# Kernel tuning notes

Measured on AMD Instinct MI355X. Metric: run time of the kernel, lower is better.

The kernel has to match this reference:

```python
import jax, jax.numpy as jnp
import numpy as np

B, T, D, H, O = 64, 512, 512, 1024, 512

def _xavier(key, shape):
    fan_out, fan_in = shape
    limit = np.sqrt(6.0 / (fan_in + fan_out))
    return jax.random.uniform(key, shape, jnp.float32, -limit, limit)

def setup_inputs() -> dict:
    key = jax.random.key(0)
    k_in, k_wx, k_wh, k_wo = jax.random.split(key, 4)
    inputs = jax.random.normal(k_in, (B, T, D), dtype=jnp.float32)
    Wx = _xavier(k_wx, (3 * H, D))   # x2h weight (n*H, D)
    bx = jnp.zeros((3 * H,), jnp.float32)
    Wh = _xavier(k_wh, (3 * H, H))   # h2h weight (n*H, H)
    bh = jnp.zeros((3 * H,), jnp.float32)
    Wo = _xavier(k_wo, (O, H))       # output head
    bo = jnp.zeros((O,), jnp.float32)
    return {"inputs": inputs, "Wx": Wx, "bx": bx, "Wh": Wh, "bh": bh, "Wo": Wo, "bo": bo}

def _gru(inputs, Wx, bx, Wh, bh):
    # precompute input projection for all timesteps: (B, T, 3H)
    x_all = jnp.einsum('btd,gd->btg', inputs, Wx) + bx

    def step(h, x_t):
        # h: (B, H); x_t: (B, 3H)
        h_proj = h @ Wh.T + bh                  # (B, 3H)
        x_r, x_u, x_n = jnp.split(x_t, 3, axis=-1)
        h_r, h_u, h_n = jnp.split(h_proj, 3, axis=-1)
        reset = jax.nn.sigmoid(x_r + h_r)
        upd = jax.nn.sigmoid(x_u + h_u)
        new = jnp.tanh(x_n + reset * h_n)       # activation='tanh'
        hy = upd * h + (1.0 - upd) * new
        return hy, hy

    h0 = jnp.zeros((inputs.shape[0], Wh.shape[1]), inputs.dtype)
    _, hs = jax.lax.scan(step, h0, jnp.swapaxes(x_all, 0, 1))  # hs: (T, B, H)
    return jnp.swapaxes(hs, 0, 1)               # (B, T, H)

def reference(inputs, Wx, bx, Wh, bh, Wo, bo):
    hiddens = _gru(inputs, Wx, bx, Wh, bh)       # (B, T, H)
    out = jnp.einsum('bth,oh->bto', hiddens, Wo) + bo  # (B, T, O)
    return hiddens, out
```

## Files before the change

kernel.cpp:

```cpp
#include <hip/hip_runtime.h>
#include <hip/hip_bf16.h>

typedef __attribute__((ext_vector_type(8))) short short8;
typedef __attribute__((ext_vector_type(4))) float float4v;

__device__ __forceinline__ float bf2f(short b) {
    unsigned u = ((unsigned)(unsigned short)b) << 16;
    union { unsigned u; float f; } c; c.u = u; return c.f;
}
__device__ __forceinline__ short f2bf(float f) {
    union { float f; unsigned u; } c; c.f = f;
    unsigned r = 0x7FFFu + ((c.u >> 16) & 1u);
    return (short)((c.u + r) >> 16);
}
__device__ __forceinline__ float ldf(const void* p, size_t i, bool f32) {
    return f32 ? ((const float*)p)[i] : bf2f(((const short*)p)[i]);
}
__device__ __forceinline__ short8 frag8(const void* p, size_t i, bool f32) {
    short8 r;
    if (f32) {
        const float* q = (const float*)p + i;
#pragma unroll
        for (int j = 0; j < 8; j++) r[j] = f2bf(q[j]);
    } else {
        r = *(const short8*)((const short*)p + i);
    }
    return r;
}

__global__ __launch_bounds__(256) void dpm_spin(const float* __restrict__ seed,
                                               float* __restrict__ sink, int iters)
{
    float a = seed[threadIdx.x & 15];
    float b = seed[(threadIdx.x & 15) + 16];
    a = (a > 2.f || a < -2.f || (a < 0.01f && a > -0.01f)) ? 1.0000001f : a;
    float x = b + 1.f;
    int n = iters * 16;
#pragma unroll 16
    for (int i = 0; i < n; i++) x = __builtin_fmaf(x, a, b);
    if (x == 12345.6789f) sink[(((size_t)blockIdx.x * 256 + threadIdx.x) & 65535)] = x;
}

__global__ void detect_dtype(const unsigned short* __restrict__ in, unsigned* __restrict__ flag)
{
    int t = threadIdx.x;
    int sane = 0;
    for (int i = t; i < 256; i += 64) {
        unsigned e = (in[i] >> 7) & 0xFF;
        sane += (e >= 0x70 && e <= 0x8A) ? 1 : 0;
    }
#pragma unroll
    for (int o = 32; o > 0; o >>= 1) sane += __shfl_down(sane, o);
    if (t == 0) *flag = (sane >= 200) ? 0u : 1u;
}

__global__ void init_scratch(short* __restrict__ hb, unsigned* __restrict__ cnt)
{
    int i = blockIdx.x * 256 + threadIdx.x;
    if (i < 4 * 65536) hb[i] = 0;
    if (i < 512) cnt[i] = 0;
}

__global__ __launch_bounds__(256, 1) void gemm_bt(
    const void* __restrict__ A, const void* __restrict__ B,
    const void* __restrict__ bias, void* __restrict__ outbase, size_t coff,
    const unsigned* __restrict__ flag, int M, int N, int K)
{
    const bool f32 = flag && (flag[0] != 0u);
    __shared__ short Ah[128][72], Bh[128][72];
    __shared__ short Al[128][72], Bl[128][72];
    const int tid  = threadIdx.x;
    const int wid  = tid >> 6;
    const int lane = tid & 63;
    const int ln = lane & 15, q = lane >> 4;
    const int bm = blockIdx.x * 128, bn = blockIdx.y * 128;
    const int wm = (wid & 1) * 64, wn = (wid >> 1) * 64;

    float4v acc[4][4];
#pragma unroll
    for (int i = 0; i < 4; i++)
#pragma unroll
        for (int j = 0; j < 4; j++) acc[i][j] = (float4v){0.f, 0.f, 0.f, 0.f};

    for (int k0 = 0; k0 < K; k0 += 64) {
#pragma unroll
        for (int c = 0; c < 4; c++) {
            int chunk = tid + c * 256;
            int row = chunk >> 3;
            int kq  = (chunk & 7) * 8;
            size_t ga = (size_t)(bm + row) * K + k0 + kq;
            size_t gb = (size_t)(bn + row) * K + k0 + kq;
            if (f32) {
                const float* Af = (const float*)A;
                const float* Bf = (const float*)B;
#pragma unroll
                for (int j = 0; j < 8; j++) {
                    float av = Af[ga + j], bv = Bf[gb + j];
                    short ah = f2bf(av), bh = f2bf(bv);
                    Ah[row][kq + j] = ah; Al[row][kq + j] = f2bf(av - bf2f(ah));
                    Bh[row][kq + j] = bh; Bl[row][kq + j] = f2bf(bv - bf2f(bh));
                }
            } else {
                *(short8*)&Ah[row][kq] = *(const short8*)((const short*)A + ga);
                *(short8*)&Bh[row][kq] = *(const short8*)((const short*)B + gb);
            }
        }
        __syncthreads();
#pragma unroll
        for (int kt = 0; kt < 2; kt++) {
            short8 avh[4], bvh[4];
#pragma unroll
            for (int i = 0; i < 4; i++) avh[i] = *(const short8*)&Ah[wm + i * 16 + ln][kt * 32 + q * 8];
#pragma unroll
            for (int j = 0; j < 4; j++) bvh[j] = *(const short8*)&Bh[wn + j * 16 + ln][kt * 32 + q * 8];
#pragma unroll
            for (int i = 0; i < 4; i++)
#pragma unroll
                for (int j = 0; j < 4; j++)
                    acc[i][j] = __builtin_amdgcn_mfma_f32_16x16x32_bf16(avh[i], bvh[j], acc[i][j], 0, 0, 0);
            if (f32) {
                short8 avl[4], bvl[4];
#pragma unroll
                for (int i = 0; i < 4; i++) avl[i] = *(const short8*)&Al[wm + i * 16 + ln][kt * 32 + q * 8];
#pragma unroll
                for (int j = 0; j < 4; j++) bvl[j] = *(const short8*)&Bl[wn + j * 16 + ln][kt * 32 + q * 8];
#pragma unroll
                for (int i = 0; i < 4; i++)
#pragma unroll
                    for (int j = 0; j < 4; j++) {
                        acc[i][j] = __builtin_amdgcn_mfma_f32_16x16x32_bf16(avh[i], bvl[j], acc[i][j], 0, 0, 0);
                        acc[i][j] = __builtin_amdgcn_mfma_f32_16x16x32_bf16(avl[i], bvh[j], acc[i][j], 0, 0, 0);
                    }
            }
        }
        __syncthreads();
    }
#pragma unroll
    for (int j = 0; j < 4; j++) {
        int col = bn + wn + j * 16 + ln;
        float bvv = ldf(bias, col, f32);
#pragma unroll
        for (int i = 0; i < 4; i++) {
#pragma unroll
            for (int r = 0; r < 4; r++) {
                int row = bm + wm + i * 16 + q * 4 + r;
                size_t idx = coff + (size_t)row * N + col;
                float v = acc[i][j][r] + bvv;
                if (f32) ((float*)outbase)[idx] = v;
                else     ((short*)outbase)[idx] = f2bf(v);
            }
        }
    }
}

#define NWG 256
__global__ __launch_bounds__(192, 1) void gru_rec(
    const void* __restrict__ inputs,
    const void* __restrict__ Wx,
    const void* __restrict__ bx,
    const void* __restrict__ Wh,
    const void* __restrict__ bh,
    short* __restrict__ hb,
    unsigned* __restrict__ cnt,
    const unsigned* __restrict__ flag,
    void* __restrict__ hid)
{
    const bool f32 = flag && (flag[0] != 0u);
    __shared__ short xs[8192];
    __shared__ short hs[2][16384];
    __shared__ float Px[3][16][17];
    __shared__ float Ph[3][16][17];
    __shared__ float hown[16][17];
    __shared__ float bxs[3][16], bhs[3][16];

    const int tid  = threadIdx.x;
    const int w    = blockIdx.x;
    const int gb   = w >> 6;
    const int c    = w & 63;
    const int g    = tid >> 6;
    const int lane = tid & 63;
    const int ln   = lane & 15, q = lane >> 4;

    const size_t whbase = (size_t)(g * 1024 + c * 16 + ln) * 1024;
    short8 wf[32];
#pragma unroll
    for (int kt = 0; kt < 32; kt++) wf[kt] = frag8(Wh, whbase + kt * 32 + q * 8, f32);

    const size_t wxbase = (size_t)(g * 1024 + c * 16 + ln) * 512;
    short8 wxf[16];
#pragma unroll
    for (int kt = 0; kt < 16; kt++) wxf[kt] = frag8(Wx, wxbase + kt * 32 + q * 8, f32);

    for (int e = tid; e < 256; e += 192) hown[e >> 4][e & 15] = 0.f;
    if (tid < 48) {
        int gg = tid >> 4, jj = tid & 15;
        bxs[gg][jj] = ldf(bx, gg * 1024 + c * 16 + jj, f32);
        bhs[gg][jj] = ldf(bh, gg * 1024 + c * 16 + jj, f32);
    }
    __syncthreads();

    for (int t = 0; t < 512; t++) {
        const short* hsrc = hb + (size_t)((t & 1) ? 2 : 0) * 65536 + gb * 16384;
        short*       hdst = hb + (size_t)((t & 1) ? 0 : 2) * 65536 + gb * 16384;

        float4v ax = (float4v){0.f,0.f,0.f,0.f};
        float4v ah = (float4v){0.f,0.f,0.f,0.f};

        unsigned long long rv[11][2];
        auto load_chunk = [&](int pl) {
            const short* src_ = hsrc + pl * 65536;
#pragma unroll
            for (int i = 0; i < 11; i++) { int e = tid + i * 192; if (e < 2048) {
                const unsigned long long* p_ = (const unsigned long long*)(src_ + e * 8);
                rv[i][0] = __hip_atomic_load(p_,     __ATOMIC_RELAXED, __HIP_MEMORY_SCOPE_AGENT);
                rv[i][1] = __hip_atomic_load(p_ + 1, __ATOMIC_RELAXED, __HIP_MEMORY_SCOPE_AGENT);
            } }
        };
        auto write_chunk = [&](int d) {
#pragma unroll
            for (int i = 0; i < 11; i++) { int e = tid + i * 192; if (e < 2048) {
                int kb = e >> 4, r = e & 15;
                union { unsigned long long qq[2]; short8 v; } u_;
                u_.qq[0] = rv[i][0]; u_.qq[1] = rv[i][1];
                *(short8*)((char*)&hs[d][0] + (kb << 8) + ((r ^ (kb & 15)) << 4)) = u_.v;
            } }
        };

#pragma unroll 4
        for (int i = 0; i < 6; i++) { int e = tid + i * 192; if (e < 1024) {
            int kb = e & 63, r = e >> 6;
            size_t gi = (size_t)(gb * 16 + r) * 262144 + (size_t)t * 512 + kb * 8;
            short8 v = frag8(inputs, gi, f32);
            *(short8*)((char*)xs + (kb << 8) + ((r ^ (kb & 15)) << 4)) = v;
        } }
        __syncthreads();

        if (t) {
            if (tid < 64) {
                const unsigned* fp = &cnt[((t - 1) & 1) * 256 + gb * 64 + tid];
                while (__hip_atomic_load(fp, __ATOMIC_RELAXED, __HIP_MEMORY_SCOPE_AGENT) < (unsigned)t)
                    __builtin_amdgcn_s_sleep(2);
            }
            __syncthreads();
        }

        load_chunk(0);
#pragma unroll
        for (int kt = 0; kt < 16; kt++) {
            int kb = kt * 4 + q;
            short8 a = *(const short8*)((const char*)xs + (kb << 8) + ((ln ^ (kb & 15)) << 4));
            ax = __builtin_amdgcn_mfma_f32_16x16x32_bf16(a, wxf[kt], ax, 0, 0, 0);
        }
        write_chunk(0);
        __syncthreads();

        load_chunk(1);
#pragma unroll
        for (int kt = 0; kt < 32; kt++) {
            int kb = kt * 4 + q;
            short8 a = *(const short8*)((const char*)&hs[0][0] + (kb << 8) + ((ln ^ (kb & 15)) << 4));
            ah = __builtin_amdgcn_mfma_f32_16x16x32_bf16(a, wf[kt], ah, 0, 0, 0);
        }
        write_chunk(1);
        __syncthreads();
#pragma unroll
        for (int kt = 0; kt < 32; kt++) {
            int kb = kt * 4 + q;
            short8 a = *(const short8*)((const char*)&hs[1][0] + (kb << 8) + ((ln ^ (kb & 15)) << 4));
            ah = __builtin_amdgcn_mfma_f32_16x16x32_bf16(a, wf[kt], ah, 0, 0, 0);
        }

#pragma unroll
        for (int r = 0; r < 4; r++) {
            Px[g][q * 4 + r][ln] = ax[r];
            Ph[g][q * 4 + r][ln] = ah[r];
        }
        __syncthreads();

        for (int e = tid; e < 256; e += 192) {
            int r = e >> 4, jj = e & 15;
            float xr = Px[0][r][jj] + bxs[0][jj];
            float xu = Px[1][r][jj] + bxs[1][jj];
            float xn = Px[2][r][jj] + bxs[2][jj];
            float pr = Ph[0][r][jj] + bhs[0][jj];
            float pu = Ph[1][r][jj] + bhs[1][jj];
            float pn = Ph[2][r][jj] + bhs[2][jj];
            float rg = 1.f / (1.f + __expf(-(xr + pr)));
            float ug = 1.f / (1.f + __expf(-(xu + pu)));
            float ng = tanhf(xn + rg * pn);
            float hy = ug * hown[r][jj] + (1.f - ug) * ng;
            hown[r][jj] = hy;
            size_t b = (size_t)(gb * 16 + r);
            size_t hidx = (b * 512 + t) * 1024 + c * 16 + jj;
            if (f32) ((float*)hid)[hidx] = hy;
            else     ((short*)hid)[hidx] = f2bf(hy);
        }
        __syncthreads();

        if (tid < 64) {
            int r = tid & 15, kbl = (tid >> 4) & 1, pl = (tid >> 5) & 1;
            union { unsigned long long qq[2]; short8 v; } u;
#pragma unroll
            for (int j = 0; j < 8; j++) {
                float hy = hown[r][kbl * 8 + j];
                short hh = f2bf(hy);
                u.v[j] = pl ? f2bf(hy - bf2f(hh)) : hh;
            }
            unsigned long long* dp = (unsigned long long*)
                (hdst + (size_t)pl * 65536 + (size_t)(2 * c + kbl) * 128 + r * 8);
            __hip_atomic_store(dp,     u.qq[0], __ATOMIC_RELAXED, __HIP_MEMORY_SCOPE_AGENT);
            __hip_atomic_store(dp + 1, u.qq[1], __ATOMIC_RELAXED, __HIP_MEMORY_SCOPE_AGENT);
        }
        asm volatile("s_waitcnt vmcnt(0)" ::: "memory");
        __syncthreads();

        if (tid == 0)
            __hip_atomic_store(&cnt[(t & 1) * 256 + gb * 64 + c], (unsigned)(t + 1),
                               __ATOMIC_RELAXED, __HIP_MEMORY_SCOPE_AGENT);
    }
}

extern "C" void kernel_launch(void* const* d_in, const int* in_sizes, int n_in,
                              void* d_out, int out_size, void* d_ws, size_t ws_size,
                              hipStream_t stream)
{
    const void* inputs = d_in[0];
    const void* Wx     = d_in[1];
    const void* bx     = d_in[2];
    const void* Wh     = d_in[3];
    const void* bh     = d_in[4];
    const void* Wo     = d_in[5];
    const void* bo     = d_in[6];

    const size_t HID_ELEMS = (size_t)64 * 512 * 1024;

    short* hb; unsigned* cnt; unsigned* flag;
    const bool use_ws = (d_ws != nullptr) && (ws_size >= (size_t)(4096 + 4 * 65536 * 2));
    if (use_ws) {
        cnt  = (unsigned*)d_ws;
        flag = cnt + 512;
        hb   = (short*)((char*)d_ws + 4096);
    } else {
        short* outh = (short*)d_out + HID_ELEMS;
        hb   = outh;
        cnt  = (unsigned*)(outh + 4 * 65536);
        flag = nullptr;
    }

    if (use_ws) detect_dtype<<<1, 64, 0, stream>>>((const unsigned short*)inputs, flag);
    init_scratch<<<1024, 256, 0, stream>>>(hb, cnt);

    gru_rec<<<NWG, 192, 0, stream>>>(inputs, Wx, bx, Wh, bh, hb, cnt, flag, d_out);

    dpm_spin<<<2048, 256, 0, stream>>>((const float*)Wx, (float*)hb, 7032);

    gemm_bt<<<dim3(256, 4), 256, 0, stream>>>(d_out, Wo, bo, d_out, HID_ELEMS, flag, 32768, 512, 1024);
}
```

Before: 5.791 ms.

## Split GRU recurrence across 512 workgroups with 8 batch rows each and drop the spin kernel

The persistent recurrent kernel now gives each workgroup 8 batch rows instead of 16 and launches 512 workgroups, two per CU. The aim is more parallel resources per timestep and less LDS per block. Barriers are consolidated: the x-tile load and the peer-wait share one barrier, and the h chunks are loaded once into registers. A single counter buffer replaces the double-buffered one, and the trailing barrier before the flag store is removed. The unrelated dummy FMA spin kernel launched between the recurrence and the output GEMM is deleted. Risks: the 16-row MFMAs now carry half-padded rows, and all 512 workgroups must be co-resident for the spin-wait synchronization to make progress.

```diff
diff --git a/kernel.cpp b/kernel.cpp
--- a/kernel.cpp
+++ b/kernel.cpp
@@ -20,25 +20,14 @@
     short8 r;
     if (f32) {
         const float* q = (const float*)p + i;
-#pragma unroll
-        for (int j = 0; j < 8; j++) r[j] = f2bf(q[j]);
+        float4v a = *(const float4v*)q;
+        float4v b = *(const float4v*)(q + 4);
+#pragma unroll
+        for (int j = 0; j < 4; j++) { r[j] = f2bf(a[j]); r[4 + j] = f2bf(b[j]); }
     } else {
         r = *(const short8*)((const short*)p + i);
     }
     return r;
-}
-
-__global__ __launch_bounds__(256) void dpm_spin(const float* __restrict__ seed,
-                                               float* __restrict__ sink, int iters)
-{
-    float a = seed[threadIdx.x & 15];
-    float b = seed[(threadIdx.x & 15) + 16];
-    a = (a > 2.f || a < -2.f || (a < 0.01f && a > -0.01f)) ? 1.0000001f : a;
-    float x = b + 1.f;
-    int n = iters * 16;
-#pragma unroll 16
-    for (int i = 0; i < n; i++) x = __builtin_fmaf(x, a, b);
-    if (x == 12345.6789f) sink[(((size_t)blockIdx.x * 256 + threadIdx.x) & 65535)] = x;
 }
 
 __global__ void detect_dtype(const unsigned short* __restrict__ in, unsigned* __restrict__ flag)
@@ -153,8 +142,8 @@
     }
 }
 
-#define NWG 256
-__global__ __launch_bounds__(192, 1) void gru_rec(
+#define NWG 512
+__global__ __launch_bounds__(192, 2) void gru_rec(
     const void* __restrict__ inputs,
     const void* __restrict__ Wx,
     const void* __restrict__ bx,
@@ -166,11 +155,11 @@
     void* __restrict__ hid)
 {
     const bool f32 = flag && (flag[0] != 0u);
-    __shared__ short xs[8192];
-    __shared__ short hs[2][16384];
-    __shared__ float Px[3][16][17];
-    __shared__ float Ph[3][16][17];
-    __shared__ float hown[16][17];
+    __shared__ short xs[4096];
+    __shared__ short hs[2][8192];
+    __shared__ float Px[3][8][17];
+    __shared__ float Ph[3][8][17];
+    __shared__ float hown[8][17];
     __shared__ float bxs[3][16], bhs[3][16];
 
     const int tid  = threadIdx.x;
@@ -180,6 +169,7 @@
     const int g    = tid >> 6;
     const int lane = tid & 63;
     const int ln   = lane & 15, q = lane >> 4;
+    const int lr   = ln & 7;
 
     const size_t whbase = (size_t)(g * 1024 + c * 16 + ln) * 1024;
     short8 wf[32];
@@ -191,7 +181,7 @@
 #pragma unroll
     for (int kt = 0; kt < 16; kt++) wxf[kt] = frag8(Wx, wxbase + kt * 32 + q * 8, f32);
 
-    for (int e = tid; e < 256; e += 192) hown[e >> 4][e & 15] = 0.f;
+    if (tid < 128) hown[tid >> 4][tid & 15] = 0.f;
     if (tid < 48) {
         int gg = tid >> 4, jj = tid & 15;
         bxs[gg][jj] = ldf(bx, gg * 1024 + c * 16 + jj, f32);
@@ -200,85 +190,72 @@
     __syncthreads();
 
     for (int t = 0; t < 512; t++) {
-        const short* hsrc = hb + (size_t)((t & 1) ? 2 : 0) * 65536 + gb * 16384;
-        short*       hdst = hb + (size_t)((t & 1) ? 0 : 2) * 65536 + gb * 16384;
+        const short* hsrc = hb + (size_t)(t & 1) * 131072 + gb * 8192;
+        short*       hdst = hb + (size_t)((t & 1) ^ 1) * 131072 + gb * 8192;
 
         float4v ax = (float4v){0.f,0.f,0.f,0.f};
         float4v ah = (float4v){0.f,0.f,0.f,0.f};
 
+#pragma unroll
+        for (int i = 0; i < 3; i++) { int e = tid + i * 192; if (e < 512) {
+            int kb = e & 63, r = e >> 6;
+            size_t gi = (size_t)(gb * 8 + r) * 262144 + (size_t)t * 512 + kb * 8;
+            short8 v = frag8(inputs, gi, f32);
+            *(short8*)((char*)xs + kb * 128 + ((r ^ (kb & 7)) << 4)) = v;
+        } }
+
+        if (t && tid < 64) {
+            const unsigned* fp = &cnt[gb * 64 + tid];
+            while (__hip_atomic_load(fp, __ATOMIC_RELAXED, __HIP_MEMORY_SCOPE_AGENT) < (unsigned)t)
+                __builtin_amdgcn_s_sleep(2);
+        }
+        __syncthreads();
+
         unsigned long long rv[11][2];
-        auto load_chunk = [&](int pl) {
-            const short* src_ = hsrc + pl * 65536;
-#pragma unroll
-            for (int i = 0; i < 11; i++) { int e = tid + i * 192; if (e < 2048) {
-                const unsigned long long* p_ = (const unsigned long long*)(src_ + e * 8);
-                rv[i][0] = __hip_atomic_load(p_,     __ATOMIC_RELAXED, __HIP_MEMORY_SCOPE_AGENT);
-                rv[i][1] = __hip_atomic_load(p_ + 1, __ATOMIC_RELAXED, __HIP_MEMORY_SCOPE_AGENT);
-            } }
-        };
-        auto write_chunk = [&](int d) {
-#pragma unroll
-            for (int i = 0; i < 11; i++) { int e = tid + i * 192; if (e < 2048) {
-                int kb = e >> 4, r = e & 15;
-                union { unsigned long long qq[2]; short8 v; } u_;
-                u_.qq[0] = rv[i][0]; u_.qq[1] = rv[i][1];
-                *(short8*)((char*)&hs[d][0] + (kb << 8) + ((r ^ (kb & 15)) << 4)) = u_.v;
-            } }
-        };
-
-#pragma unroll 4
-        for (int i = 0; i < 6; i++) { int e = tid + i * 192; if (e < 1024) {
-            int kb = e & 63, r = e >> 6;
-            size_t gi = (size_t)(gb * 16 + r) * 262144 + (size_t)t * 512 + kb * 8;
-            short8 v = frag8(inputs, gi, f32);
-            *(short8*)((char*)xs + (kb << 8) + ((r ^ (kb & 15)) << 4)) = v;
+#pragma unroll
+        for (int i = 0; i < 11; i++) { int e = tid + i * 192; if (e < 2048) {
+            const unsigned long long* p_ = (const unsigned long long*)
+                (hsrc + (size_t)(e >> 10) * 65536 + (size_t)(e & 1023) * 8);
+            rv[i][0] = __hip_atomic_load(p_,     __ATOMIC_RELAXED, __HIP_MEMORY_SCOPE_AGENT);
+            rv[i][1] = __hip_atomic_load(p_ + 1, __ATOMIC_RELAXED, __HIP_MEMORY_SCOPE_AGENT);
         } }
-        __syncthreads();
-
-        if (t) {
-            if (tid < 64) {
-                const unsigned* fp = &cnt[((t - 1) & 1) * 256 + gb * 64 + tid];
-                while (__hip_atomic_load(fp, __ATOMIC_RELAXED, __HIP_MEMORY_SCOPE_AGENT) < (unsigned)t)
-                    __builtin_amdgcn_s_sleep(2);
-            }
-            __syncthreads();
-        }
-
-        load_chunk(0);
+
 #pragma unroll
         for (int kt = 0; kt < 16; kt++) {
             int kb = kt * 4 + q;
-            short8 a = *(const short8*)((const char*)xs + (kb << 8) + ((ln ^ (kb & 15)) << 4));
+            short8 a = *(const short8*)((const char*)xs + kb * 128 + ((lr ^ (kb & 7)) << 4));
             ax = __builtin_amdgcn_mfma_f32_16x16x32_bf16(a, wxf[kt], ax, 0, 0, 0);
         }
-        write_chunk(0);
-        __syncthreads();
-
-        load_chunk(1);
-#pragma unroll
-        for (int kt = 0; kt < 32; kt++) {
-            int kb = kt * 4 + q;
-            short8 a = *(const short8*)((const char*)&hs[0][0] + (kb << 8) + ((ln ^ (kb & 15)) << 4));
-            ah = __builtin_amdgcn_mfma_f32_16x16x32_bf16(a, wf[kt], ah, 0, 0, 0);
-        }
-        write_chunk(1);
-        __syncthreads();
-#pragma unroll
-        for (int kt = 0; kt < 32; kt++) {
-            int kb = kt * 4 + q;
-            short8 a = *(const short8*)((const char*)&hs[1][0] + (kb << 8) + ((ln ^ (kb & 15)) << 4));
-            ah = __builtin_amdgcn_mfma_f32_16x16x32_bf16(a, wf[kt], ah, 0, 0, 0);
-        }
-
-#pragma unroll
-        for (int r = 0; r < 4; r++) {
-            Px[g][q * 4 + r][ln] = ax[r];
-            Ph[g][q * 4 + r][ln] = ah[r];
-        }
-        __syncthreads();
-
-        for (int e = tid; e < 256; e += 192) {
-            int r = e >> 4, jj = e & 15;
+
+#pragma unroll
+        for (int i = 0; i < 11; i++) { int e = tid + i * 192; if (e < 2048) {
+            int pl = e >> 10, u = e & 1023, kb = u >> 3, r = u & 7;
+            union { unsigned long long qq[2]; short8 v; } u_;
+            u_.qq[0] = rv[i][0]; u_.qq[1] = rv[i][1];
+            *(short8*)((char*)&hs[pl][0] + kb * 128 + ((r ^ (kb & 7)) << 4)) = u_.v;
+        } }
+        __syncthreads();
+
+#pragma unroll
+        for (int pl = 0; pl < 2; pl++)
+#pragma unroll
+            for (int kt = 0; kt < 32; kt++) {
+                int kb = kt * 4 + q;
+                short8 a = *(const short8*)((const char*)&hs[pl][0] + kb * 128 + ((lr ^ (kb & 7)) << 4));
+                ah = __builtin_amdgcn_mfma_f32_16x16x32_bf16(a, wf[kt], ah, 0, 0, 0);
+            }
+
+        if (q < 2) {
+#pragma unroll
+            for (int r = 0; r < 4; r++) {
+                Px[g][q * 4 + r][ln] = ax[r];
+                Ph[g][q * 4 + r][ln] = ah[r];
+            }
+        }
+        __syncthreads();
+
+        if (tid < 128) {
+            int r = tid >> 4, jj = tid & 15;
             float xr = Px[0][r][jj] + bxs[0][jj];
             float xu = Px[1][r][jj] + bxs[1][jj];
             float xn = Px[2][r][jj] + bxs[2][jj];
@@ -290,15 +267,15 @@
             float ng = tanhf(xn + rg * pn);
             float hy = ug * hown[r][jj] + (1.f - ug) * ng;
             hown[r][jj] = hy;
-            size_t b = (size_t)(gb * 16 + r);
+            size_t b = (size_t)(gb * 8 + r);
             size_t hidx = (b * 512 + t) * 1024 + c * 16 + jj;
             if (f32) ((float*)hid)[hidx] = hy;
             else     ((short*)hid)[hidx] = f2bf(hy);
         }
         __syncthreads();
 
-        if (tid < 64) {
-            int r = tid & 15, kbl = (tid >> 4) & 1, pl = (tid >> 5) & 1;
+        if (tid < 32) {
+            int r = tid & 7, kbl = (tid >> 3) & 1, pl = tid >> 4;
             union { unsigned long long qq[2]; short8 v; } u;
 #pragma unroll
             for (int j = 0; j < 8; j++) {
@@ -307,15 +284,14 @@
                 u.v[j] = pl ? f2bf(hy - bf2f(hh)) : hh;
             }
             unsigned long long* dp = (unsigned long long*)
-                (hdst + (size_t)pl * 65536 + (size_t)(2 * c + kbl) * 128 + r * 8);
+                (hdst + (size_t)pl * 65536 + (size_t)(2 * c + kbl) * 64 + r * 8);
             __hip_atomic_store(dp,     u.qq[0], __ATOMIC_RELAXED, __HIP_MEMORY_SCOPE_AGENT);
             __hip_atomic_store(dp + 1, u.qq[1], __ATOMIC_RELAXED, __HIP_MEMORY_SCOPE_AGENT);
         }
         asm volatile("s_waitcnt vmcnt(0)" ::: "memory");
-        __syncthreads();
 
         if (tid == 0)
-            __hip_atomic_store(&cnt[(t & 1) * 256 + gb * 64 + c], (unsigned)(t + 1),
+            __hip_atomic_store(&cnt[gb * 64 + c], (unsigned)(t + 1),
                                __ATOMIC_RELAXED, __HIP_MEMORY_SCOPE_AGENT);
     }
 }
@@ -352,7 +328,5 @@
 
     gru_rec<<<NWG, 192, 0, stream>>>(inputs, Wx, bx, Wh, bh, hb, cnt, flag, d_out);
 
-    dpm_spin<<<2048, 256, 0, stream>>>((const float*)Wx, (float*)hb, 7032);
-
     gemm_bt<<<dim3(256, 4), 256, 0, stream>>>(d_out, Wo, bo, d_out, HID_ELEMS, flag, 32768, 512, 1024);
 }
```

Result: slower. 8.048 ms (+39.0%).
